# Performance work log

Hardware: AMD Instinct MI355X
Metric: run time of the kernel (lower is better)

The kernel has to match this reference:

```python
import jax, jax.numpy as jnp
import numpy as np

HEADS = 4
DIM_U = 1
DIM_K = 16
DIM_V = 32  # dim_out // heads = 128 // 4
EPS = 1e-5


def setup_inputs() -> dict:
    key = jax.random.key(0)
    ks = jax.random.split(key, 9)
    b, dim, hh, ww = 16, 256, 32, 32
    n = m = hh * ww
    x = jax.random.normal(ks[0], (b, dim, hh, ww), dtype=jnp.float32)
    # 1x1 conv weights (out_ch, in_ch), kaiming-ish scale
    s = 1.0 / np.sqrt(dim)
    w_q = jax.random.normal(ks[1], (DIM_K * HEADS, dim), dtype=jnp.float32) * s
    w_k = jax.random.normal(ks[2], (DIM_K * DIM_U, dim), dtype=jnp.float32) * s
    w_v = jax.random.normal(ks[3], (DIM_V * DIM_U, dim), dtype=jnp.float32) * s
    pos_emb = jax.random.normal(ks[4], (n, m, DIM_K, DIM_U), dtype=jnp.float32)
    gamma_q = jnp.ones((DIM_K * HEADS,), dtype=jnp.float32)
    beta_q = jnp.zeros((DIM_K * HEADS,), dtype=jnp.float32)
    gamma_v = jnp.ones((DIM_V * DIM_U,), dtype=jnp.float32)
    beta_v = jnp.zeros((DIM_V * DIM_U,), dtype=jnp.float32)
    return {"x": x, "w_q": w_q, "w_k": w_k, "w_v": w_v, "pos_emb": pos_emb,
            "gamma_q": gamma_q, "beta_q": beta_q, "gamma_v": gamma_v, "beta_v": beta_v}


def _bn(t, gamma, beta):
    # BatchNorm2d in training mode: batch statistics over (b, h, w), biased var
    mean = t.mean(axis=(0, 2, 3), keepdims=True)
    var = t.var(axis=(0, 2, 3), keepdims=True)
    t = (t - mean) * jax.lax.rsqrt(var + EPS)
    return t * gamma[None, :, None, None] + beta[None, :, None, None]


def reference(x, w_q, w_k, w_v, pos_emb, gamma_q, beta_q, gamma_v, beta_v):
    b, c, hh, ww = x.shape
    h, u, dk, dv = HEADS, DIM_U, DIM_K, DIM_V
    # 1x1 convs == channel contractions
    q = jnp.einsum('oc,bcxy->boxy', w_q, x)
    k = jnp.einsum('oc,bcxy->boxy', w_k, x)
    v = jnp.einsum('oc,bcxy->boxy', w_v, x)
    q = _bn(q, gamma_q, beta_q)
    v = _bn(v, gamma_v, beta_v)
    n = hh * ww
    q = q.reshape(b, h, dk, n)        # b h k n
    k = k.reshape(b, dk, u, n)        # b k u m
    v = v.reshape(b, dv, u, n)        # b v u m
    k = jax.nn.softmax(k, axis=-1)
    lam_c = jnp.einsum('bkum,bvum->bkv', k, v)            # content lambda
    lam_p = jnp.einsum('nmku,bvum->bnkv', pos_emb, v)     # position lambdas
    Yc = jnp.einsum('bhkn,bkv->bnhv', q, lam_c)
    Yp = jnp.einsum('bhkn,bnkv->bnhv', q, lam_p)
    Y = Yc + Yp                                           # b n h v
    out = Y.transpose(0, 2, 3, 1).reshape(b, h * dv, hh, ww)
    return out
```

## Files before the change

### kernel.cpp

```cpp
#include <hip/hip_runtime.h>
#include <hip/hip_bf16.h>
#include <cstdint>


typedef __attribute__((ext_vector_type(8))) __bf16 bf16x8;
typedef __attribute__((ext_vector_type(4))) float f32x4;

__device__ __forceinline__ unsigned short f2bf(float f) {
    unsigned u = __float_as_uint(f);
    u += 0x7fffu + ((u >> 16) & 1u);
    return (unsigned short)(u >> 16);
}
__device__ __forceinline__ float bf2f(unsigned short h) {
    return __uint_as_float(((unsigned)h) << 16);
}
__device__ __forceinline__ void async16(const void* g, void* l) {
    __builtin_amdgcn_global_load_lds(
        (const __attribute__((address_space(1))) void*)g,
        (__attribute__((address_space(3))) void*)l, 16, 0, 0);
}

__global__ __launch_bounds__(256) void k_transp(const float* __restrict__ pos,
                                                unsigned* __restrict__ PbfU,
                                                const float* __restrict__ wq,
                                                const float* __restrict__ wk,
                                                const float* __restrict__ wv,
                                                unsigned* __restrict__ WbfU) {
    int blk = blockIdx.x;
    int t = threadIdx.x;
    if (blk >= 1024) {
        int tt = (blk - 1024) * 256 + t;
#pragma unroll
        for (int r = 0; r < 4; ++r) {
            int u = r * 4096 + tt;
            int row = u >> 7;
            int cp = (u & 127) << 1;
            float f0 = 0.f, f1 = 0.f;
            if (row < 64)       { f0 = wq[row * 256 + cp];        f1 = wq[row * 256 + cp + 1]; }
            else if (row < 80)  { f0 = wk[(row - 64) * 256 + cp]; f1 = wk[(row - 64) * 256 + cp + 1]; }
            else if (row < 112) { f0 = wv[(row - 80) * 256 + cp]; f1 = wv[(row - 80) * 256 + cp + 1]; }
            WbfU[u] = (unsigned)f2bf(f0) | ((unsigned)f2bf(f1) << 16);
        }
        return;
    }
    __shared__ __align__(16) unsigned short L[16 * 1032];
    const float4* src = (const float4*)(pos + (size_t)blk * 16384);
#pragma unroll
    for (int r = 0; r < 16; ++r) {
        int idx4 = r * 256 + t;
        float4 f = src[idx4];
        int m = idx4 >> 2, k0 = (idx4 & 3) << 2;
        L[(k0 + 0) * 1032 + m] = f2bf(f.x);
        L[(k0 + 1) * 1032 + m] = f2bf(f.y);
        L[(k0 + 2) * 1032 + m] = f2bf(f.z);
        L[(k0 + 3) * 1032 + m] = f2bf(f.w);
    }
    __syncthreads();
    uint2* dst = (uint2*)(PbfU + (size_t)blk * 8192);
#pragma unroll
    for (int r = 0; r < 16; ++r) {
        int c = r * 256 + t;
        int k = c >> 8, mo = c & 255;
        dst[c] = *(const uint2*)&L[k * 1032 + mo * 4];
    }
}

__global__ __launch_bounds__(256) void k_proj(const float* __restrict__ x,
                                              const unsigned short* __restrict__ Wbf,
                                              float* __restrict__ qraw,
                                              float* __restrict__ kraw,
                                              float* __restrict__ vraw) {
    int b = blockIdx.y;
    int px0 = blockIdx.x * 64;
    int t = threadIdx.x;
    int w = t >> 6, lane = t & 63;

    __shared__ __align__(16) unsigned short Al[128 * 32];
    __shared__ __align__(16) unsigned short Bl[64 * 34];

    int srow = (w << 5) + (lane >> 2);
    int schunk = (lane & 3) ^ ((lane >> 3) & 3);
    const unsigned short* pA0 = Wbf + srow * 256 + schunk * 8;
    const unsigned short* pA1 = pA0 + 16 * 256;
    unsigned short* lA0 = &Al[w * 1024];
    unsigned short* lA1 = lA0 + 512;

    int wm = w >> 1, wn = w & 1;
    int rl = lane & 15, qq = lane >> 4;
    int sw = qq ^ ((rl >> 1) & 3);

    f32x4 acc[4][2];
#pragma unroll
    for (int i = 0; i < 4; ++i)
#pragma unroll
        for (int j = 0; j < 2; ++j)
#pragma unroll
            for (int r = 0; r < 4; ++r) acc[i][j][r] = 0.f;

    const float* xb = x + (size_t)b * 256 * 1024 + px0;

    for (int kt = 0; kt < 8; ++kt) {
        int c0 = kt * 32;
        async16(pA0 + c0, lA0);
        async16(pA1 + c0, lA1);
#pragma unroll
        for (int rep = 0; rep < 4; ++rep) {
            int idx = rep * 256 + t;
            int px = idx & 63;
            int cp = idx >> 6;
            int c = c0 + cp * 2;
            float f0 = xb[(size_t)c * 1024 + px];
            float f1 = xb[(size_t)(c + 1) * 1024 + px];
            *(unsigned*)&Bl[px * 34 + cp * 2] = (unsigned)f2bf(f0) | ((unsigned)f2bf(f1) << 16);
        }
        __syncthreads();
        bf16x8 a[4], bb[2];
#pragma unroll
        for (int i = 0; i < 4; ++i) a[i]  = *(const bf16x8*)&Al[((wm << 6) + (i << 4) + rl) * 32 + sw * 8];
#pragma unroll
        for (int j = 0; j < 2; ++j) bb[j] = *(const bf16x8*)&Bl[((wn << 5) + (j << 4) + rl) * 34 + qq * 8];
#pragma unroll
        for (int i = 0; i < 4; ++i)
#pragma unroll
            for (int j = 0; j < 2; ++j)
                acc[i][j] = __builtin_amdgcn_mfma_f32_16x16x32_bf16(a[i], bb[j], acc[i][j], 0, 0, 0);
        __syncthreads();
    }

#pragma unroll
    for (int i = 0; i < 4; ++i) {
#pragma unroll
        for (int j = 0; j < 2; ++j) {
            int px = px0 + (wn << 5) + (j << 4) + (lane & 15);
#pragma unroll
            for (int r = 0; r < 4; ++r) {
                int ch = (wm << 6) + (i << 4) + ((lane >> 4) << 2) + r;
                float val = acc[i][j][r];
                if (ch < 64)       qraw[((size_t)b * 64 + ch) * 1024 + px] = val;
                else if (ch < 80)  kraw[((size_t)b * 16 + (ch - 64)) * 1024 + px] = val;
                else if (ch < 112) vraw[((size_t)b * 32 + (ch - 80)) * 1024 + px] = val;
            }
        }
    }
}

__global__ __launch_bounds__(1024) void k_stats(const float* __restrict__ qraw,
                                                const float* __restrict__ vraw,
                                                const float* __restrict__ gq, const float* __restrict__ bq,
                                                const float* __restrict__ gv, const float* __restrict__ bv,
                                                float* __restrict__ scaleArr, float* __restrict__ shiftArr) {
    int ch = blockIdx.x;
    int t = threadIdx.x;
    const float* base;
    size_t bstride;
    if (ch < 64) { base = qraw + (size_t)ch * 1024; bstride = 64 * 1024; }
    else         { base = vraw + (size_t)(ch - 64) * 1024; bstride = 32 * 1024; }
    float s = 0.f, ss = 0.f;
#pragma unroll
    for (int b = 0; b < 16; ++b) { float v = base[b * bstride + t]; s += v; ss += v * v; }
#pragma unroll
    for (int off = 32; off; off >>= 1) { s += __shfl_down(s, off); ss += __shfl_down(ss, off); }
    __shared__ float rs[16], rss[16];
    if ((t & 63) == 0) { rs[t >> 6] = s; rss[t >> 6] = ss; }
    __syncthreads();
    if (t == 0) {
        s = 0.f; ss = 0.f;
#pragma unroll
        for (int i = 0; i < 16; ++i) { s += rs[i]; ss += rss[i]; }
        float mean = s * (1.f / 16384.f);
        float var = ss * (1.f / 16384.f) - mean * mean;
        float g, be;
        if (ch < 64) { g = gq[ch]; be = bq[ch]; } else { g = gv[ch - 64]; be = bv[ch - 64]; }
        float sc = g * rsqrtf(var + 1e-5f);
        scaleArr[ch] = sc;
        shiftArr[ch] = be - mean * sc;
    }
}

__global__ void k_bn(const float* __restrict__ qraw, const float* __restrict__ vraw,
                     const float* __restrict__ scaleArr, const float* __restrict__ shiftArr,
                     float* __restrict__ qbn, unsigned* __restrict__ vbnU) {
    int bx = blockIdx.x;
    int t = threadIdx.x;
    if (bx < 256) {
        int nt = bx & 15, b = bx >> 4;
        __shared__ float Q[64 * 65];
        const float* src = qraw + (size_t)b * 64 * 1024 + nt * 64;
#pragma unroll
        for (int r = 0; r < 16; ++r) {
            int idx = r * 256 + t; int ch = idx >> 6; int nl = idx & 63;
            Q[ch * 65 + nl] = src[(size_t)ch * 1024 + nl];
        }
        __syncthreads();
        float* dst = qbn + ((size_t)b * 1024 + nt * 64) * 64;
#pragma unroll
        for (int r = 0; r < 16; ++r) {
            int idx = r * 256 + t; int nl = idx >> 6; int ch = idx & 63;
            dst[(size_t)nl * 64 + ch] = Q[ch * 65 + nl] * scaleArr[ch] + shiftArr[ch];
        }
    } else {
        int tt = (bx - 256) * 256 + t;
#pragma unroll
        for (int r = 0; r < 4; ++r) {
            int u = r * 65536 + tt;
            int row = u >> 9;
            int vch = row & 31;
            float sc = scaleArr[64 + vch], sh = shiftArr[64 + vch];
            float f0 = vraw[2 * u] * sc + sh;
            float f1 = vraw[2 * u + 1] * sc + sh;
            vbnU[u] = (unsigned)f2bf(f0) | ((unsigned)f2bf(f1) << 16);
        }
    }
}

__global__ void k_sm_lamc(const float* __restrict__ kraw, const unsigned short* __restrict__ vbn,
                          float* __restrict__ lamc) {
    int kch = blockIdx.x, b = blockIdx.y;
    int t = threadIdx.x; int w = t >> 6; int lane = t & 63;
    const float* kr = kraw + ((size_t)b * 16 + kch) * 1024;
    float xv[4];
    float mx = -1e30f;
#pragma unroll
    for (int i = 0; i < 4; ++i) { xv[i] = kr[t + i * 256]; mx = fmaxf(mx, xv[i]); }
#pragma unroll
    for (int off = 32; off; off >>= 1) mx = fmaxf(mx, __shfl_down(mx, off));
    __shared__ float red[4];
    __shared__ float pr[4][32];
    if (lane == 0) red[w] = mx;
    __syncthreads();
    mx = fmaxf(fmaxf(red[0], red[1]), fmaxf(red[2], red[3]));
    float e[4]; float s = 0.f;
#pragma unroll
    for (int i = 0; i < 4; ++i) { e[i] = __expf(xv[i] - mx); s += e[i]; }
#pragma unroll
    for (int off = 32; off; off >>= 1) s += __shfl_down(s, off);
    __syncthreads();
    if (lane == 0) red[w] = s;
    __syncthreads();
    float inv = 1.f / (red[0] + red[1] + red[2] + red[3]);
    const unsigned short* vb = vbn + (size_t)b * 32 * 1024;
    for (int vch = 0; vch < 32; ++vch) {
        const unsigned short* vr = vb + (size_t)vch * 1024;
        float p = 0.f;
#pragma unroll
        for (int i = 0; i < 4; ++i) p += e[i] * bf2f(vr[t + i * 256]);
#pragma unroll
        for (int off = 32; off; off >>= 1) p += __shfl_down(p, off);
        if (lane == 0) pr[w][vch] = p;
    }
    __syncthreads();
    if (t < 32) {
        float tot = pr[0][t] + pr[1][t] + pr[2][t] + pr[3][t];
        lamc[((size_t)b * 16 + kch) * 32 + t] = inv * tot;
    }
}

__global__ __launch_bounds__(256, 4) void k_lamp(const unsigned short* __restrict__ Pbf,
                                                 const unsigned short* __restrict__ vbn,
                                                 const float* __restrict__ qbn,
                                                 const float* __restrict__ lamc,
                                                 float* __restrict__ out) {
    int mtile = blockIdx.x;
    int ntile = blockIdx.y;
    int t = threadIdx.x;
    int w = t >> 6, lane = t & 63;

    __shared__ union {
        struct { __align__(16) unsigned short A[8192]; __align__(16) unsigned short B[8192]; } st;
        unsigned short Ybf[128 * 132];
    } sm;

    int srow = t >> 3;
    int jx = (t & 7) ^ (srow & 7);
    const unsigned short* pA = Pbf + ((size_t)(mtile * 128) + srow) * 1024 + jx * 8;
    const unsigned short* pB = vbn + ((size_t)(ntile * 128) + srow) * 1024 + jx * 8;
    unsigned short* ldsA = &sm.st.A[t * 8];
    unsigned short* ldsB = &sm.st.B[t * 8];

    int wm = w >> 1, wn = w & 1;
    int rl = lane & 15, qq = lane >> 4;
    int abase[2], bbase[2];
#pragma unroll
    for (int ks = 0; ks < 2; ++ks) {
        abase[ks] = (wm * 64 + rl) * 64 + (((ks * 4 + qq) ^ (rl & 7)) << 3);
        bbase[ks] = (wn * 64 + rl) * 64 + (((ks * 4 + qq) ^ (rl & 7)) << 3);
    }

    f32x4 acc[4][4];
#pragma unroll
    for (int i = 0; i < 4; ++i)
#pragma unroll
        for (int j = 0; j < 4; ++j)
#pragma unroll
            for (int r = 0; r < 4; ++r) acc[i][j][r] = 0.f;

    for (int kt = 0; kt < 16; ++kt) {
        int m0 = kt * 64;
#pragma unroll
        for (int i = 0; i < 4; ++i) {
            async16(pA + (size_t)i * 32 * 1024 + m0, ldsA + i * 2048);
            async16(pB + (size_t)i * 32 * 1024 + m0, ldsB + i * 2048);
        }
        __syncthreads();
#pragma unroll
        for (int ks = 0; ks < 2; ++ks) {
            bf16x8 a[4], bb[4];
#pragma unroll
            for (int i = 0; i < 4; ++i) a[i]  = *(const bf16x8*)&sm.st.A[abase[ks] + i * 1024];
#pragma unroll
            for (int j = 0; j < 4; ++j) bb[j] = *(const bf16x8*)&sm.st.B[bbase[ks] + j * 1024];
#pragma unroll
            for (int i = 0; i < 4; ++i)
#pragma unroll
                for (int j = 0; j < 4; ++j)
                    acc[i][j] = __builtin_amdgcn_mfma_f32_16x16x32_bf16(a[i], bb[j], acc[i][j], 0, 0, 0);
        }
        __syncthreads();
    }

    int b0 = ntile * 4;
#pragma unroll
    for (int i = 0; i < 4; ++i) {
        int row_b = (wm << 6) + (i << 4) + (qq << 2);
#pragma unroll
        for (int j = 0; j < 4; ++j) {
            int col = (wn << 6) + (j << 4) + rl;
            int bcol = col >> 5, vv = col & 31;
            const float* lc = lamc + ((size_t)(b0 + bcol) * 16) * 32 + vv;
#pragma unroll
            for (int r = 0; r < 4; ++r) {
                int row = row_b + r;
                sm.Ybf[row * 132 + col] = f2bf(acc[i][j][r] + lc[(row & 15) * 32]);
            }
        }
    }
    __syncthreads();

    int c0 = t * 2;
    int bb2 = c0 >> 7;
    int hh = (c0 >> 5) & 3;
    int v0 = c0 & 31;
    int bglob = b0 + bb2;
    float o0[8], o1[8];
#pragma unroll
    for (int nn = 0; nn < 8; ++nn) { o0[nn] = 0.f; o1[nn] = 0.f; }
    const float* qb = qbn + ((size_t)bglob * 1024 + mtile * 8) * 64 + hh * 16;
#pragma unroll
    for (int nn = 0; nn < 8; ++nn) {
        const float* qr = qb + nn * 64;
        float qv[16];
        *(float4*)&qv[0]  = *(const float4*)&qr[0];
        *(float4*)&qv[4]  = *(const float4*)&qr[4];
        *(float4*)&qv[8]  = *(const float4*)&qr[8];
        *(float4*)&qv[12] = *(const float4*)&qr[12];
        const unsigned short* yrow = &sm.Ybf[(nn * 16) * 132 + bb2 * 32 + v0];
#pragma unroll
        for (int k = 0; k < 16; ++k) {
            float y0 = bf2f(yrow[k * 132]);
            float y1 = bf2f(yrow[k * 132 + 1]);
            o0[nn] += qv[k] * y0;
            o1[nn] += qv[k] * y1;
        }
    }
    float* op = out + ((size_t)bglob * 128 + hh * 32 + v0) * 1024 + mtile * 8;
    ((float4*)op)[0] = make_float4(o0[0], o0[1], o0[2], o0[3]);
    ((float4*)op)[1] = make_float4(o0[4], o0[5], o0[6], o0[7]);
    float* op1 = op + 1024;
    ((float4*)op1)[0] = make_float4(o1[0], o1[1], o1[2], o1[3]);
    ((float4*)op1)[1] = make_float4(o1[4], o1[5], o1[6], o1[7]);
}

extern "C" void kernel_launch(void* const* d_in, const int* in_sizes, int n_in,
                              void* d_out, int out_size, void* d_ws, size_t ws_size,
                              hipStream_t stream) {
    const float* x   = (const float*)d_in[0];
    const float* wq  = (const float*)d_in[1];
    const float* wk  = (const float*)d_in[2];
    const float* wv  = (const float*)d_in[3];
    const float* pos = (const float*)d_in[4];
    const float* gq  = (const float*)d_in[5];
    const float* bq  = (const float*)d_in[6];
    const float* gv  = (const float*)d_in[7];
    const float* bv  = (const float*)d_in[8];
    float* out = (float*)d_out;

    char* ws = (char*)d_ws;
    unsigned short* Pbf  = (unsigned short*)(ws);
    unsigned short* Wbf  = (unsigned short*)(ws + 33554432);
    float* qraw          = (float*)(ws + 33619968);
    float* kraw          = (float*)(ws + 37814272);
    float* vraw          = (float*)(ws + 38862848);
    float* qbn           = (float*)(ws + 40960000);
    unsigned short* vbn  = (unsigned short*)(ws + 45154304);
    float* scaleArr      = (float*)(ws + 46202880);
    float* shiftArr      = (float*)(ws + 46203392);
    float* lamc          = (float*)(ws + 46203904);

    k_transp<<<dim3(1040), dim3(256), 0, stream>>>(pos, (unsigned*)Pbf, wq, wk, wv, (unsigned*)Wbf);
    k_proj<<<dim3(16, 16), dim3(256), 0, stream>>>(x, Wbf, qraw, kraw, vraw);
    k_stats<<<dim3(96), dim3(1024), 0, stream>>>(qraw, vraw, gq, bq, gv, bv, scaleArr, shiftArr);
    k_bn<<<dim3(512), dim3(256), 0, stream>>>(qraw, vraw, scaleArr, shiftArr, qbn, (unsigned*)vbn);
    k_sm_lamc<<<dim3(16, 16), dim3(256), 0, stream>>>(kraw, vbn, lamc);
    k_lamp<<<dim3(128, 4), dim3(256), 0, stream>>>(Pbf, vbn, qbn, lamc, out);
}
```

Before: 188.7 us.

## Fuse pos_emb conversion into lambda kernel and merge BN, stats, softmax stages

Removes the separate pos_emb transpose/bf16 pass: k_lamp now reads fp32 pos_emb directly, converts it to bf16 and writes it swizzled into LDS. The q BatchNorm is applied inside the output epilogue, and lamc is computed from raw v with the v affine folded in afterwards. Stats, v normalisation and the content lambda are merged into one launch, which cuts launches and drops the 32MB bf16 round trip and the qbn buffer. In exchange the pos load becomes synchronous register loads rather than async LDS copies, and k_proj uses smaller tiles with weights converted on every block.

After: 208.2 us. +10.3%, slower.

```diff
diff --git a/kernel.cpp b/kernel.cpp
--- a/kernel.cpp
+++ b/kernel.cpp
@@ -11,6 +11,9 @@
     u += 0x7fffu + ((u >> 16) & 1u);
     return (unsigned short)(u >> 16);
 }
+__device__ __forceinline__ unsigned pk2(float a, float b) {
+    return (unsigned)f2bf(a) | ((unsigned)f2bf(b) << 16);
+}
 __device__ __forceinline__ float bf2f(unsigned short h) {
     return __uint_as_float(((unsigned)h) << 16);
 }
@@ -20,245 +23,194 @@
         (__attribute__((address_space(3))) void*)l, 16, 0, 0);
 }
 
-__global__ __launch_bounds__(256) void k_transp(const float* __restrict__ pos,
-                                                unsigned* __restrict__ PbfU,
-                                                const float* __restrict__ wq,
-                                                const float* __restrict__ wk,
-                                                const float* __restrict__ wv,
-                                                unsigned* __restrict__ WbfU) {
-    int blk = blockIdx.x;
-    int t = threadIdx.x;
-    if (blk >= 1024) {
-        int tt = (blk - 1024) * 256 + t;
-#pragma unroll
-        for (int r = 0; r < 4; ++r) {
-            int u = r * 4096 + tt;
-            int row = u >> 7;
-            int cp = (u & 127) << 1;
-            float f0 = 0.f, f1 = 0.f;
-            if (row < 64)       { f0 = wq[row * 256 + cp];        f1 = wq[row * 256 + cp + 1]; }
-            else if (row < 80)  { f0 = wk[(row - 64) * 256 + cp]; f1 = wk[(row - 64) * 256 + cp + 1]; }
-            else if (row < 112) { f0 = wv[(row - 80) * 256 + cp]; f1 = wv[(row - 80) * 256 + cp + 1]; }
-            WbfU[u] = (unsigned)f2bf(f0) | ((unsigned)f2bf(f1) << 16);
-        }
-        return;
-    }
-    __shared__ __align__(16) unsigned short L[16 * 1032];
-    const float4* src = (const float4*)(pos + (size_t)blk * 16384);
-#pragma unroll
-    for (int r = 0; r < 16; ++r) {
-        int idx4 = r * 256 + t;
-        float4 f = src[idx4];
-        int m = idx4 >> 2, k0 = (idx4 & 3) << 2;
-        L[(k0 + 0) * 1032 + m] = f2bf(f.x);
-        L[(k0 + 1) * 1032 + m] = f2bf(f.y);
-        L[(k0 + 2) * 1032 + m] = f2bf(f.z);
-        L[(k0 + 3) * 1032 + m] = f2bf(f.w);
-    }
-    __syncthreads();
-    uint2* dst = (uint2*)(PbfU + (size_t)blk * 8192);
-#pragma unroll
-    for (int r = 0; r < 16; ++r) {
-        int c = r * 256 + t;
-        int k = c >> 8, mo = c & 255;
-        dst[c] = *(const uint2*)&L[k * 1032 + mo * 4];
-    }
-}
-
 __global__ __launch_bounds__(256) void k_proj(const float* __restrict__ x,
-                                              const unsigned short* __restrict__ Wbf,
+                                              const float* __restrict__ wq,
+                                              const float* __restrict__ wk,
+                                              const float* __restrict__ wv,
                                               float* __restrict__ qraw,
                                               float* __restrict__ kraw,
                                               float* __restrict__ vraw) {
     int b = blockIdx.y;
-    int px0 = blockIdx.x * 64;
+    int px0 = blockIdx.x * 32;
     int t = threadIdx.x;
     int w = t >> 6, lane = t & 63;
 
     __shared__ __align__(16) unsigned short Al[128 * 32];
-    __shared__ __align__(16) unsigned short Bl[64 * 34];
-
-    int srow = (w << 5) + (lane >> 2);
-    int schunk = (lane & 3) ^ ((lane >> 3) & 3);
-    const unsigned short* pA0 = Wbf + srow * 256 + schunk * 8;
-    const unsigned short* pA1 = pA0 + 16 * 256;
-    unsigned short* lA0 = &Al[w * 1024];
-    unsigned short* lA1 = lA0 + 512;
+    __shared__ __align__(16) unsigned short Bl[32 * 34];
+
+    int ch = t >> 1, half = t & 1;
+    const float* wsrc = nullptr;
+    if (ch < 64)       wsrc = wq + ch * 256;
+    else if (ch < 80)  wsrc = wk + (ch - 64) * 256;
+    else if (ch < 112) wsrc = wv + (ch - 80) * 256;
+    if (wsrc) wsrc += half * 16;
+    int s2 = (ch >> 1) & 3;
+    unsigned short* wdst0 = &Al[ch * 32 + (((half * 2) ^ s2) << 3)];
+    unsigned short* wdst1 = &Al[ch * 32 + (((half * 2 + 1) ^ s2) << 3)];
 
     int wm = w >> 1, wn = w & 1;
     int rl = lane & 15, qq = lane >> 4;
     int sw = qq ^ ((rl >> 1) & 3);
 
-    f32x4 acc[4][2];
+    f32x4 acc[4];
 #pragma unroll
     for (int i = 0; i < 4; ++i)
 #pragma unroll
-        for (int j = 0; j < 2; ++j)
-#pragma unroll
-            for (int r = 0; r < 4; ++r) acc[i][j][r] = 0.f;
-
-    const float* xb = x + (size_t)b * 256 * 1024 + px0;
+        for (int r = 0; r < 4; ++r) acc[i][r] = 0.f;
+
+    const float* xb = x + (size_t)b * 262144 + px0;
 
     for (int kt = 0; kt < 8; ++kt) {
         int c0 = kt * 32;
-        async16(pA0 + c0, lA0);
-        async16(pA1 + c0, lA1);
-#pragma unroll
-        for (int rep = 0; rep < 4; ++rep) {
+        {
+            uint4 d0, d1;
+            if (wsrc) {
+                float4 f0 = *(const float4*)(wsrc + c0);
+                float4 f1 = *(const float4*)(wsrc + c0 + 4);
+                float4 f2 = *(const float4*)(wsrc + c0 + 8);
+                float4 f3 = *(const float4*)(wsrc + c0 + 12);
+                d0.x = pk2(f0.x, f0.y); d0.y = pk2(f0.z, f0.w);
+                d0.z = pk2(f1.x, f1.y); d0.w = pk2(f1.z, f1.w);
+                d1.x = pk2(f2.x, f2.y); d1.y = pk2(f2.z, f2.w);
+                d1.z = pk2(f3.x, f3.y); d1.w = pk2(f3.z, f3.w);
+            } else {
+                d0 = make_uint4(0, 0, 0, 0); d1 = d0;
+            }
+            *(uint4*)wdst0 = d0;
+            *(uint4*)wdst1 = d1;
+        }
+#pragma unroll
+        for (int rep = 0; rep < 2; ++rep) {
             int idx = rep * 256 + t;
-            int px = idx & 63;
-            int cp = idx >> 6;
+            int px = idx & 31;
+            int cp = idx >> 5;
             int c = c0 + cp * 2;
             float f0 = xb[(size_t)c * 1024 + px];
             float f1 = xb[(size_t)(c + 1) * 1024 + px];
-            *(unsigned*)&Bl[px * 34 + cp * 2] = (unsigned)f2bf(f0) | ((unsigned)f2bf(f1) << 16);
-        }
-        __syncthreads();
-        bf16x8 a[4], bb[2];
-#pragma unroll
-        for (int i = 0; i < 4; ++i) a[i]  = *(const bf16x8*)&Al[((wm << 6) + (i << 4) + rl) * 32 + sw * 8];
-#pragma unroll
-        for (int j = 0; j < 2; ++j) bb[j] = *(const bf16x8*)&Bl[((wn << 5) + (j << 4) + rl) * 34 + qq * 8];
+            *(unsigned*)&Bl[px * 34 + cp * 2] = pk2(f0, f1);
+        }
+        __syncthreads();
+        bf16x8 a[4], bb;
+#pragma unroll
+        for (int i = 0; i < 4; ++i) a[i] = *(const bf16x8*)&Al[((wm << 6) + (i << 4) + rl) * 32 + sw * 8];
+        bb = *(const bf16x8*)&Bl[((wn << 4) + rl) * 34 + qq * 8];
 #pragma unroll
         for (int i = 0; i < 4; ++i)
-#pragma unroll
-            for (int j = 0; j < 2; ++j)
-                acc[i][j] = __builtin_amdgcn_mfma_f32_16x16x32_bf16(a[i], bb[j], acc[i][j], 0, 0, 0);
+            acc[i] = __builtin_amdgcn_mfma_f32_16x16x32_bf16(a[i], bb, acc[i], 0, 0, 0);
         __syncthreads();
     }
 
 #pragma unroll
     for (int i = 0; i < 4; ++i) {
-#pragma unroll
-        for (int j = 0; j < 2; ++j) {
-            int px = px0 + (wn << 5) + (j << 4) + (lane & 15);
-#pragma unroll
-            for (int r = 0; r < 4; ++r) {
-                int ch = (wm << 6) + (i << 4) + ((lane >> 4) << 2) + r;
-                float val = acc[i][j][r];
-                if (ch < 64)       qraw[((size_t)b * 64 + ch) * 1024 + px] = val;
-                else if (ch < 80)  kraw[((size_t)b * 16 + (ch - 64)) * 1024 + px] = val;
-                else if (ch < 112) vraw[((size_t)b * 32 + (ch - 80)) * 1024 + px] = val;
-            }
-        }
-    }
-}
-
-__global__ __launch_bounds__(1024) void k_stats(const float* __restrict__ qraw,
-                                                const float* __restrict__ vraw,
-                                                const float* __restrict__ gq, const float* __restrict__ bq,
-                                                const float* __restrict__ gv, const float* __restrict__ bv,
-                                                float* __restrict__ scaleArr, float* __restrict__ shiftArr) {
-    int ch = blockIdx.x;
-    int t = threadIdx.x;
-    const float* base;
-    size_t bstride;
-    if (ch < 64) { base = qraw + (size_t)ch * 1024; bstride = 64 * 1024; }
-    else         { base = vraw + (size_t)(ch - 64) * 1024; bstride = 32 * 1024; }
-    float s = 0.f, ss = 0.f;
-#pragma unroll
-    for (int b = 0; b < 16; ++b) { float v = base[b * bstride + t]; s += v; ss += v * v; }
-#pragma unroll
-    for (int off = 32; off; off >>= 1) { s += __shfl_down(s, off); ss += __shfl_down(ss, off); }
-    __shared__ float rs[16], rss[16];
-    if ((t & 63) == 0) { rs[t >> 6] = s; rss[t >> 6] = ss; }
-    __syncthreads();
-    if (t == 0) {
-        s = 0.f; ss = 0.f;
-#pragma unroll
-        for (int i = 0; i < 16; ++i) { s += rs[i]; ss += rss[i]; }
-        float mean = s * (1.f / 16384.f);
-        float var = ss * (1.f / 16384.f) - mean * mean;
-        float g, be;
-        if (ch < 64) { g = gq[ch]; be = bq[ch]; } else { g = gv[ch - 64]; be = bv[ch - 64]; }
-        float sc = g * rsqrtf(var + 1e-5f);
-        scaleArr[ch] = sc;
-        shiftArr[ch] = be - mean * sc;
-    }
-}
-
-__global__ void k_bn(const float* __restrict__ qraw, const float* __restrict__ vraw,
-                     const float* __restrict__ scaleArr, const float* __restrict__ shiftArr,
-                     float* __restrict__ qbn, unsigned* __restrict__ vbnU) {
+        int px = px0 + (wn << 4) + rl;
+#pragma unroll
+        for (int r = 0; r < 4; ++r) {
+            int c = (wm << 6) + (i << 4) + (qq << 2) + r;
+            float val = acc[i][r];
+            if (c < 64)       qraw[((size_t)b * 64 + c) * 1024 + px] = val;
+            else if (c < 80)  kraw[((size_t)b * 16 + (c - 64)) * 1024 + px] = val;
+            else if (c < 112) vraw[((size_t)b * 32 + (c - 80)) * 1024 + px] = val;
+        }
+    }
+}
+
+__global__ __launch_bounds__(1024) void k_mid(const float* __restrict__ qraw,
+                                              const float* __restrict__ kraw,
+                                              const float* __restrict__ vraw,
+                                              const float* __restrict__ gq, const float* __restrict__ bq,
+                                              const float* __restrict__ gv, const float* __restrict__ bv,
+                                              unsigned short* __restrict__ vbn,
+                                              float* __restrict__ scaleArr, float* __restrict__ shiftArr,
+                                              float* __restrict__ lamcraw) {
     int bx = blockIdx.x;
     int t = threadIdx.x;
-    if (bx < 256) {
-        int nt = bx & 15, b = bx >> 4;
-        __shared__ float Q[64 * 65];
-        const float* src = qraw + (size_t)b * 64 * 1024 + nt * 64;
-#pragma unroll
-        for (int r = 0; r < 16; ++r) {
-            int idx = r * 256 + t; int ch = idx >> 6; int nl = idx & 63;
-            Q[ch * 65 + nl] = src[(size_t)ch * 1024 + nl];
-        }
-        __syncthreads();
-        float* dst = qbn + ((size_t)b * 1024 + nt * 64) * 64;
-#pragma unroll
-        for (int r = 0; r < 16; ++r) {
-            int idx = r * 256 + t; int nl = idx >> 6; int ch = idx & 63;
-            dst[(size_t)nl * 64 + ch] = Q[ch * 65 + nl] * scaleArr[ch] + shiftArr[ch];
+    int w = t >> 6, lane = t & 63;
+    __shared__ float redA[16], redB[16];
+    __shared__ float bc[2];
+    __shared__ float pr[16][32];
+
+    if (bx < 96) {
+        int ch = bx;
+        const float* base;
+        size_t bstride;
+        if (ch < 64) { base = qraw + (size_t)ch * 1024; bstride = 65536; }
+        else         { base = vraw + (size_t)(ch - 64) * 1024; bstride = 32768; }
+        float s = 0.f, ss = 0.f;
+#pragma unroll
+        for (int b = 0; b < 16; ++b) { float v = base[b * bstride + t]; s += v; ss += v * v; }
+#pragma unroll
+        for (int off = 32; off; off >>= 1) { s += __shfl_down(s, off); ss += __shfl_down(ss, off); }
+        if (lane == 0) { redA[w] = s; redB[w] = ss; }
+        __syncthreads();
+        if (t == 0) {
+            s = 0.f; ss = 0.f;
+#pragma unroll
+            for (int i = 0; i < 16; ++i) { s += redA[i]; ss += redB[i]; }
+            float mean = s * (1.f / 16384.f);
+            float var = ss * (1.f / 16384.f) - mean * mean;
+            float g, be;
+            if (ch < 64) { g = gq[ch]; be = bq[ch]; } else { g = gv[ch - 64]; be = bv[ch - 64]; }
+            float sc = g * rsqrtf(var + 1e-5f);
+            float sh = be - mean * sc;
+            scaleArr[ch] = sc; shiftArr[ch] = sh;
+            bc[0] = sc; bc[1] = sh;
+        }
+        __syncthreads();
+        if (ch >= 64) {
+            float sc = bc[0], sh = bc[1];
+            int vch = ch - 64;
+#pragma unroll
+            for (int b = 0; b < 16; ++b) {
+                size_t idx = ((size_t)b * 32 + vch) * 1024 + t;
+                vbn[idx] = f2bf(vraw[idx] * sc + sh);
+            }
         }
     } else {
-        int tt = (bx - 256) * 256 + t;
-#pragma unroll
-        for (int r = 0; r < 4; ++r) {
-            int u = r * 65536 + tt;
-            int row = u >> 9;
-            int vch = row & 31;
-            float sc = scaleArr[64 + vch], sh = shiftArr[64 + vch];
-            float f0 = vraw[2 * u] * sc + sh;
-            float f1 = vraw[2 * u + 1] * sc + sh;
-            vbnU[u] = (unsigned)f2bf(f0) | ((unsigned)f2bf(f1) << 16);
-        }
-    }
-}
-
-__global__ void k_sm_lamc(const float* __restrict__ kraw, const unsigned short* __restrict__ vbn,
-                          float* __restrict__ lamc) {
-    int kch = blockIdx.x, b = blockIdx.y;
-    int t = threadIdx.x; int w = t >> 6; int lane = t & 63;
-    const float* kr = kraw + ((size_t)b * 16 + kch) * 1024;
-    float xv[4];
-    float mx = -1e30f;
-#pragma unroll
-    for (int i = 0; i < 4; ++i) { xv[i] = kr[t + i * 256]; mx = fmaxf(mx, xv[i]); }
-#pragma unroll
-    for (int off = 32; off; off >>= 1) mx = fmaxf(mx, __shfl_down(mx, off));
-    __shared__ float red[4];
-    __shared__ float pr[4][32];
-    if (lane == 0) red[w] = mx;
-    __syncthreads();
-    mx = fmaxf(fmaxf(red[0], red[1]), fmaxf(red[2], red[3]));
-    float e[4]; float s = 0.f;
-#pragma unroll
-    for (int i = 0; i < 4; ++i) { e[i] = __expf(xv[i] - mx); s += e[i]; }
-#pragma unroll
-    for (int off = 32; off; off >>= 1) s += __shfl_down(s, off);
-    __syncthreads();
-    if (lane == 0) red[w] = s;
-    __syncthreads();
-    float inv = 1.f / (red[0] + red[1] + red[2] + red[3]);
-    const unsigned short* vb = vbn + (size_t)b * 32 * 1024;
-    for (int vch = 0; vch < 32; ++vch) {
-        const unsigned short* vr = vb + (size_t)vch * 1024;
-        float p = 0.f;
-#pragma unroll
-        for (int i = 0; i < 4; ++i) p += e[i] * bf2f(vr[t + i * 256]);
-#pragma unroll
-        for (int off = 32; off; off >>= 1) p += __shfl_down(p, off);
-        if (lane == 0) pr[w][vch] = p;
-    }
-    __syncthreads();
-    if (t < 32) {
-        float tot = pr[0][t] + pr[1][t] + pr[2][t] + pr[3][t];
-        lamc[((size_t)b * 16 + kch) * 32 + t] = inv * tot;
-    }
-}
-
-__global__ __launch_bounds__(256, 4) void k_lamp(const unsigned short* __restrict__ Pbf,
+        int idx = bx - 96;
+        int b = idx >> 4, kch = idx & 15;
+        float xv = kraw[((size_t)b * 16 + kch) * 1024 + t];
+        float mx = xv;
+#pragma unroll
+        for (int off = 32; off; off >>= 1) mx = fmaxf(mx, __shfl_down(mx, off));
+        if (lane == 0) redA[w] = mx;
+        __syncthreads();
+        mx = redA[0];
+#pragma unroll
+        for (int i = 1; i < 16; ++i) mx = fmaxf(mx, redA[i]);
+        float e = __expf(xv - mx);
+        float s = e;
+#pragma unroll
+        for (int off = 32; off; off >>= 1) s += __shfl_down(s, off);
+        __syncthreads();
+        if (lane == 0) redB[w] = s;
+        __syncthreads();
+        s = 0.f;
+#pragma unroll
+        for (int i = 0; i < 16; ++i) s += redB[i];
+        float inv = 1.f / s;
+        const float* vb = vraw + (size_t)b * 32768;
+        for (int v = 0; v < 32; ++v) {
+            float p = e * vb[(size_t)v * 1024 + t];
+#pragma unroll
+            for (int off = 32; off; off >>= 1) p += __shfl_down(p, off);
+            if (lane == 0) pr[w][v] = p;
+        }
+        __syncthreads();
+        if (t < 32) {
+            float tot = 0.f;
+#pragma unroll
+            for (int i = 0; i < 16; ++i) tot += pr[i][t];
+            lamcraw[((size_t)b * 16 + kch) * 32 + t] = inv * tot;
+        }
+    }
+}
+
+__global__ __launch_bounds__(256, 4) void k_lamp(const float* __restrict__ pos,
                                                  const unsigned short* __restrict__ vbn,
-                                                 const float* __restrict__ qbn,
-                                                 const float* __restrict__ lamc,
+                                                 const float* __restrict__ qraw,
+                                                 const float* __restrict__ lamcraw,
+                                                 const float* __restrict__ scaleArr,
+                                                 const float* __restrict__ shiftArr,
                                                  float* __restrict__ out) {
     int mtile = blockIdx.x;
     int ntile = blockIdx.y;
@@ -270,11 +222,14 @@
         unsigned short Ybf[128 * 132];
     } sm;
 
+    int nl = t >> 5;
+    int k0 = (t >> 3) & 3;
+    int am = t & 7;
+    const float* pAg = pos + ((size_t)(mtile * 8 + nl)) * 16384 + (size_t)am * 128 + k0 * 4;
+
     int srow = t >> 3;
     int jx = (t & 7) ^ (srow & 7);
-    const unsigned short* pA = Pbf + ((size_t)(mtile * 128) + srow) * 1024 + jx * 8;
     const unsigned short* pB = vbn + ((size_t)(ntile * 128) + srow) * 1024 + jx * 8;
-    unsigned short* ldsA = &sm.st.A[t * 8];
     unsigned short* ldsB = &sm.st.B[t * 8];
 
     int wm = w >> 1, wn = w & 1;
@@ -295,11 +250,24 @@
             for (int r = 0; r < 4; ++r) acc[i][j][r] = 0.f;
 
     for (int kt = 0; kt < 16; ++kt) {
-        int m0 = kt * 64;
-#pragma unroll
-        for (int i = 0; i < 4; ++i) {
-            async16(pA + (size_t)i * 32 * 1024 + m0, ldsA + i * 2048);
-            async16(pB + (size_t)i * 32 * 1024 + m0, ldsB + i * 2048);
+#pragma unroll
+        for (int i = 0; i < 4; ++i)
+            async16(pB + (size_t)i * 32 * 1024 + kt * 64, ldsB + i * 2048);
+        {
+            const float* ps = pAg + (size_t)kt * 1024;
+            float4 fl[8];
+#pragma unroll
+            for (int i = 0; i < 8; ++i) fl[i] = *(const float4*)(ps + i * 16);
+#pragma unroll
+            for (int c = 0; c < 4; ++c) {
+                uint4 d;
+                d.x = pk2(((const float*)&fl[0])[c], ((const float*)&fl[1])[c]);
+                d.y = pk2(((const float*)&fl[2])[c], ((const float*)&fl[3])[c]);
+                d.z = pk2(((const float*)&fl[4])[c], ((const float*)&fl[5])[c]);
+                d.w = pk2(((const float*)&fl[6])[c], ((const float*)&fl[7])[c]);
+                int row = nl * 16 + k0 * 4 + c;
+                *(uint4*)&sm.st.A[row * 64 + ((am ^ (row & 7)) << 3)] = d;
+            }
         }
         __syncthreads();
 #pragma unroll
@@ -320,17 +288,19 @@
 
     int b0 = ntile * 4;
 #pragma unroll
-    for (int i = 0; i < 4; ++i) {
-        int row_b = (wm << 6) + (i << 4) + (qq << 2);
-#pragma unroll
-        for (int j = 0; j < 4; ++j) {
-            int col = (wn << 6) + (j << 4) + rl;
-            int bcol = col >> 5, vv = col & 31;
-            const float* lc = lamc + ((size_t)(b0 + bcol) * 16) * 32 + vv;
+    for (int j = 0; j < 4; ++j) {
+        int col = (wn << 6) + (j << 4) + rl;
+        int bcol = col >> 5, vv = col & 31;
+        float scv = scaleArr[64 + vv], shv = shiftArr[64 + vv];
+        const float* lc = lamcraw + ((size_t)(b0 + bcol) * 16) * 32 + vv;
+#pragma unroll
+        for (int i = 0; i < 4; ++i) {
+            int row_b = (wm << 6) + (i << 4) + (qq << 2);
 #pragma unroll
             for (int r = 0; r < 4; ++r) {
                 int row = row_b + r;
-                sm.Ybf[row * 132 + col] = f2bf(acc[i][j][r] + lc[(row & 15) * 32]);
+                float lamc = scv * lc[(row & 15) * 32] + shv;
+                sm.Ybf[row * 132 + col] = f2bf(acc[i][j][r] + lamc);
             }
         }
     }
@@ -344,22 +314,19 @@
     float o0[8], o1[8];
 #pragma unroll
     for (int nn = 0; nn < 8; ++nn) { o0[nn] = 0.f; o1[nn] = 0.f; }
-    const float* qb = qbn + ((size_t)bglob * 1024 + mtile * 8) * 64 + hh * 16;
-#pragma unroll
-    for (int nn = 0; nn < 8; ++nn) {
-        const float* qr = qb + nn * 64;
-        float qv[16];
-        *(float4*)&qv[0]  = *(const float4*)&qr[0];
-        *(float4*)&qv[4]  = *(const float4*)&qr[4];
-        *(float4*)&qv[8]  = *(const float4*)&qr[8];
-        *(float4*)&qv[12] = *(const float4*)&qr[12];
-        const unsigned short* yrow = &sm.Ybf[(nn * 16) * 132 + bb2 * 32 + v0];
-#pragma unroll
-        for (int k = 0; k < 16; ++k) {
-            float y0 = bf2f(yrow[k * 132]);
-            float y1 = bf2f(yrow[k * 132 + 1]);
-            o0[nn] += qv[k] * y0;
-            o1[nn] += qv[k] * y1;
+    const float* qsrc = qraw + ((size_t)bglob * 64 + hh * 16) * 1024 + mtile * 8;
+#pragma unroll
+    for (int k = 0; k < 16; ++k) {
+        float4 qa = *(const float4*)(qsrc + (size_t)k * 1024);
+        float4 qb4 = *(const float4*)(qsrc + (size_t)k * 1024 + 4);
+        float sc = scaleArr[hh * 16 + k], sh = shiftArr[hh * 16 + k];
+        float qv[8] = {qa.x, qa.y, qa.z, qa.w, qb4.x, qb4.y, qb4.z, qb4.w};
+#pragma unroll
+        for (int nn = 0; nn < 8; ++nn) {
+            float qn = qv[nn] * sc + sh;
+            unsigned yp = *(const unsigned*)&sm.Ybf[(nn * 16 + k) * 132 + bb2 * 32 + v0];
+            o0[nn] += qn * bf2f((unsigned short)(yp & 0xffff));
+            o1[nn] += qn * bf2f((unsigned short)(yp >> 16));
         }
     }
     float* op = out + ((size_t)bglob * 128 + hh * 32 + v0) * 1024 + mtile * 8;
@@ -385,21 +352,17 @@
     float* out = (float*)d_out;
 
     char* ws = (char*)d_ws;
-    unsigned short* Pbf  = (unsigned short*)(ws);
-    unsigned short* Wbf  = (unsigned short*)(ws + 33554432);
-    float* qraw          = (float*)(ws + 33619968);
-    float* kraw          = (float*)(ws + 37814272);
-    float* vraw          = (float*)(ws + 38862848);
-    float* qbn           = (float*)(ws + 40960000);
-    unsigned short* vbn  = (unsigned short*)(ws + 45154304);
-    float* scaleArr      = (float*)(ws + 46202880);
-    float* shiftArr      = (float*)(ws + 46203392);
-    float* lamc          = (float*)(ws + 46203904);
-
-    k_transp<<<dim3(1040), dim3(256), 0, stream>>>(pos, (unsigned*)Pbf, wq, wk, wv, (unsigned*)Wbf);
-    k_proj<<<dim3(16, 16), dim3(256), 0, stream>>>(x, Wbf, qraw, kraw, vraw);
-    k_stats<<<dim3(96), dim3(1024), 0, stream>>>(qraw, vraw, gq, bq, gv, bv, scaleArr, shiftArr);
-    k_bn<<<dim3(512), dim3(256), 0, stream>>>(qraw, vraw, scaleArr, shiftArr, qbn, (unsigned*)vbn);
-    k_sm_lamc<<<dim3(16, 16), dim3(256), 0, stream>>>(kraw, vbn, lamc);
-    k_lamp<<<dim3(128, 4), dim3(256), 0, stream>>>(Pbf, vbn, qbn, lamc, out);
-}
+    float* qraw          = (float*)(ws);
+    float* kraw          = (float*)(ws + 4194304);
+    float* vraw          = (float*)(ws + 5242880);
+    unsigned short* vbn  = (unsigned short*)(ws + 7340032);
+    float* lamcraw       = (float*)(ws + 8388608);
+    float* scaleArr      = (float*)(ws + 8421376);
+    float* shiftArr      = (float*)(ws + 8421888);
+
+    k_proj<<<dim3(32, 16), dim3(256), 0, stream>>>(x, wq, wk, wv, qraw, kraw, vraw);
+    k_mid<<<dim3(352), dim3(1024), 0, stream>>>(qraw, kraw, vraw, gq, bq, gv, bv,
+                                                vbn, scaleArr, shiftArr, lamcraw);
+    k_lamp<<<dim3(128, 4), dim3(256), 0, stream>>>(pos, vbn, qraw, lamcraw,
+                                                   scaleArr, shiftArr, out);
+}
```
